# Performance work log

Hardware: AMD Instinct MI355X
Metric: run time of the kernel (lower is better)

## Reference

```python
import jax, jax.numpy as jnp
import numpy as np
import math

N_HEAD = 16
ROPE_BASE = 10000.0

def _rope_cos_sin(seq_len, head_dim, dtype):
    inv_freq = 1.0 / (ROPE_BASE ** (jnp.arange(0, head_dim, 2, dtype=jnp.float32) / head_dim))
    t = jnp.arange(seq_len, dtype=jnp.float32)
    freqs = t[:, None] * inv_freq[None, :]            # [S, D/2]
    emb = jnp.concatenate([freqs, freqs], axis=-1)     # [S, D]
    # broadcast shape [1, 1, S, D] to match q/k [B, H, S, D]
    return jnp.cos(emb)[None, None].astype(dtype), jnp.sin(emb)[None, None].astype(dtype)

def _rotate_half(x):
    x1, x2 = jnp.split(x, 2, axis=-1)
    return jnp.concatenate([-x2, x1], axis=-1)

def setup_inputs() -> dict:
    key = jax.random.key(0)
    ks = jax.random.split(key, 5)
    B, S, E = 2, 2048, 1024
    x = jax.random.normal(ks[0], (B, S, E), dtype=jnp.float32)
    init = 1.0 / math.sqrt(E)
    Wq = jax.random.normal(ks[1], (E, E), dtype=jnp.float32) * init
    Wk = jax.random.normal(ks[2], (E, E), dtype=jnp.float32) * init
    Wv = jax.random.normal(ks[3], (E, E), dtype=jnp.float32) * init
    Wo = jax.random.normal(ks[4], (E, E), dtype=jnp.float32) * init
    # causal mask: True = masked (masked_fill with -inf)
    attn_mask = jnp.triu(jnp.ones((S, S), dtype=bool), k=1)
    return {"x": x, "Wq": Wq, "Wk": Wk, "Wv": Wv, "Wo": Wo, "attn_mask": attn_mask}

def reference(x, Wq, Wk, Wv, Wo, attn_mask):
    B, S, E = x.shape
    H = N_HEAD
    D = E // H
    # projections (torch Linear: y = x @ W.T), split heads -> [B, H, S, D]
    def proj(W):
        return jnp.einsum('bse,fe->bsf', x, W).reshape(B, S, H, D).transpose(0, 2, 1, 3)
    q, k, v = proj(Wq), proj(Wk), proj(Wv)
    cos, sin = _rope_cos_sin(S, D, x.dtype)
    q = q * cos + _rotate_half(q) * sin
    k = k * cos + _rotate_half(k) * sin
    scale = 1.0 / math.sqrt(D)
    scores = jnp.einsum('bhqd,bhkd->bhqk', q, k) * scale  # [B, H, S, S]
    scores = jnp.where(attn_mask[None, None], -jnp.inf, scores)
    attn = jax.nn.softmax(scores, axis=-1)
    out = jnp.einsum('bhqk,bhkd->bhqd', attn, v)           # [B, H, S, D]
    out = out.transpose(0, 2, 1, 3).reshape(B, S, E)
    return jnp.einsum('bse,fe->bsf', out, Wo)
```

## Files before the change

kernel.cpp:

```cpp
#include <hip/hip_runtime.h>
#include <hip/hip_bf16.h>

#define NB 2
#define NH 16
#define SEQ 2048
#define HD 64
#define EMB 1024

typedef unsigned short u16;
typedef unsigned int u32;
typedef __attribute__((ext_vector_type(8))) short bf16x8;
typedef __attribute__((ext_vector_type(4))) float f32x4;
typedef __attribute__((ext_vector_type(8))) unsigned short us8;

__device__ __forceinline__ float b2f(u16 u) {
    union { unsigned int i; float f; } v; v.i = ((unsigned int)u) << 16; return v.f;
}
__device__ __forceinline__ u16 f2b(float f) {
    union { float f; unsigned int i; } v; v.f = f;
    unsigned int x = v.i;
    return (u16)((x + 0x7FFFu + ((x >> 16) & 1u)) >> 16);
}
__device__ __forceinline__ u32 pk2(float a, float b) {
    union { __hip_bfloat162 h; u32 u; } v;
    v.h = __float22bfloat162_rn(make_float2(a, b));
    return v.u;
}

__device__ __forceinline__ void gld16(const u16* g, u16* l) {
    __builtin_amdgcn_global_load_lds((const __attribute__((address_space(1))) void*)g,
                                     (__attribute__((address_space(3))) void*)l, 16, 0, 0);
}

__device__ __forceinline__ void conv8(const void* src, u16* dst, int i, int isbf16) {
    if (isbf16) {
        *reinterpret_cast<uint4*>(dst + i) =
            *reinterpret_cast<const uint4*>((const u16*)src + i);
    } else {
        const float* s = (const float*)src + i;
        float4 a = *reinterpret_cast<const float4*>(s);
        float4 b = *reinterpret_cast<const float4*>(s + 4);
        us8 v;
        v[0] = f2b(a.x); v[1] = f2b(a.y); v[2] = f2b(a.z); v[3] = f2b(a.w);
        v[4] = f2b(b.x); v[5] = f2b(b.y); v[6] = f2b(b.z); v[7] = f2b(b.w);
        *reinterpret_cast<us8*>(dst + i) = v;
    }
}

__global__ __launch_bounds__(256)
void prep_54571854463007(const void* __restrict__ x,
                         const void* __restrict__ w0, const void* __restrict__ w1,
                         const void* __restrict__ w2, const void* __restrict__ w3,
                         u16* __restrict__ xb, u16* __restrict__ dqkv,
                         u16* __restrict__ dob, int* __restrict__ flag) {
    __shared__ int cnt;
    if (threadIdx.x == 0) cnt = 0;
    __syncthreads();
    const u16 v = ((const u16*)x)[threadIdx.x];
    const int e = (v >> 7) & 0xFF;
    if (e >= 110 && e <= 135) atomicAdd(&cnt, 1);
    __syncthreads();
    const int isbf16 = (cnt >= 200) ? 1 : 0;
    const int blk = blockIdx.x;
    if (blk == 0 && threadIdx.x == 0) *flag = isbf16;
    const int NXB = (NB * SEQ * EMB) / 2048;
    if (blk < NXB) {
        conv8(x, xb, (blk * 256 + threadIdx.x) * 8, isbf16);
    } else {
        const int r = blk - NXB;
        const int seg = r >> 9;
        const int NW = EMB * EMB;
        const void* src = (seg == 0) ? w0 : (seg == 1) ? w1 : (seg == 2) ? w2 : w3;
        u16* dst = (seg < 3) ? (dqkv + (size_t)seg * NW) : dob;
        conv8(src, dst, ((r & 511) * 256 + threadIdx.x) * 8, isbf16);
    }
}

template<int OUT_MODE>
__global__ __launch_bounds__(256)
void gemm_mfma_54571854463007(const u16* __restrict__ A, const u16* __restrict__ Bw,
                              void* __restrict__ C, const int* __restrict__ flagp,
                              int M, int N, int K) {
    __shared__ __align__(16) u16 As[128 * 32];
    __shared__ __align__(16) u16 Bs[128 * 32];
    const int tid  = threadIdx.x;
    const int wave = tid >> 6, lane = tid & 63;
    const int quad = lane >> 4, fr = lane & 15;
    const int wr = (wave >> 1) * 64, wc = (wave & 1) * 64;
    const int m0 = blockIdx.y * 128, n0 = blockIdx.x * 128;
    const int r0 = tid >> 2;
    const int kc = (tid & 3) * 8;
    const f32x4 zz = {0.f, 0.f, 0.f, 0.f};
    f32x4 acc[4][4];
#pragma unroll
    for (int i = 0; i < 4; ++i)
#pragma unroll
        for (int j = 0; j < 4; ++j) acc[i][j] = zz;

    for (int k0 = 0; k0 < K; k0 += 32) {
        gld16(A  + (size_t)(m0 + r0) * K + k0 + kc,      &As[wave * 512]);
        gld16(A  + (size_t)(m0 + 64 + r0) * K + k0 + kc, &As[2048 + wave * 512]);
        gld16(Bw + (size_t)(n0 + r0) * K + k0 + kc,      &Bs[wave * 512]);
        gld16(Bw + (size_t)(n0 + 64 + r0) * K + k0 + kc, &Bs[2048 + wave * 512]);
        __syncthreads();
        bf16x8 af[4], bfr[4];
#pragma unroll
        for (int mi = 0; mi < 4; ++mi)
            af[mi] = *reinterpret_cast<const bf16x8*>(&As[(wr + mi * 16 + fr) * 32 + quad * 8]);
#pragma unroll
        for (int ni = 0; ni < 4; ++ni)
            bfr[ni] = *reinterpret_cast<const bf16x8*>(&Bs[(wc + ni * 16 + fr) * 32 + quad * 8]);
#pragma unroll
        for (int mi = 0; mi < 4; ++mi)
#pragma unroll
            for (int ni = 0; ni < 4; ++ni)
                acc[mi][ni] = __builtin_amdgcn_mfma_f32_16x16x32_bf16(af[mi], bfr[ni], acc[mi][ni], 0, 0, 0);
        __syncthreads();
    }

    if (OUT_MODE == 1) {
        const int t0 = n0 >> 10;
        if (t0 == 0) {
            const float SCL = 0.18033688011112042f;
#pragma unroll
            for (int mi = 0; mi < 4; ++mi)
#pragma unroll
                for (int ni = 0; ni < 4; ++ni)
#pragma unroll
                    for (int r = 0; r < 4; ++r) acc[mi][ni][r] *= SCL;
        }
        if (t0 < 2) {
            const float inv0 = __powf(10000.f, -(float)fr / 32.f);
            const float inv1 = __powf(10000.f, -(float)(fr + 16) / 32.f);
#pragma unroll
            for (int mi = 0; mi < 4; ++mi)
#pragma unroll
                for (int r = 0; r < 4; ++r) {
                    const int s = (m0 + wr + mi * 16 + quad * 4 + r) & (SEQ - 1);
#pragma unroll
                    for (int nl = 0; nl < 2; ++nl) {
                        float sn, cs;
                        __sincosf((float)s * (nl ? inv1 : inv0), &sn, &cs);
                        const float lo = acc[mi][nl][r], hi = acc[mi][nl + 2][r];
                        acc[mi][nl][r]     = lo * cs - hi * sn;
                        acc[mi][nl + 2][r] = hi * cs + lo * sn;
                    }
                }
        }
    }

    const int isbf16 = (OUT_MODE == 0) ? *flagp : 0;
    const size_t TS = (size_t)NB * NH * SEQ * HD;
#pragma unroll
    for (int mi = 0; mi < 4; ++mi)
#pragma unroll
        for (int ni = 0; ni < 4; ++ni)
#pragma unroll
            for (int r = 0; r < 4; ++r) {
                const int m = m0 + wr + mi * 16 + quad * 4 + r;
                const int n = n0 + wc + ni * 16 + fr;
                const float v = acc[mi][ni][r];
                if (OUT_MODE == 1) {
                    const int t = n >> 10, idx = n & 1023;
                    const int h = idx >> 6, d = idx & 63;
                    const int b = m >> 11, s = m & (SEQ - 1);
                    ((u16*)C)[t * TS + ((((size_t)b * NH + h) * SEQ + s) << 6) + d] = f2b(v);
                } else {
                    if (isbf16) ((u16*)C)[(size_t)m * N + n] = f2b(v);
                    else        ((float*)C)[(size_t)m * N + n] = v;
                }
            }
}

__global__ __launch_bounds__(256, 4)
void flash_54571854463007(const u16* __restrict__ Q, const u16* __restrict__ K,
                          const u16* __restrict__ V, u16* __restrict__ AO,
                          float* __restrict__ OP0, float* __restrict__ OP1,
                          float* __restrict__ LP0, float* __restrict__ LP1) {
    __shared__ __align__(16) u16 Kt[2 * 4096];
    __shared__ __align__(16) u16 Vt[2 * 4608];
    const int tid  = threadIdx.x;
    const int w    = tid >> 6, lane = tid & 63;
    const int quad = lane >> 4, fr = lane & 15;
    const int lin = blockIdx.x;
    const int xcd = lin & 7;
    const int r_  = lin >> 3;
    const int b4  = r_ & 3;
    const int ti  = r_ >> 2;
    int qt, kt0, kt1;
    if (ti < 17)       { qt = 15 + ti; kt0 = 0;  kt1 = 15; }
    else if (ti == 17) { qt = 31;      kt0 = 16; kt1 = 31; }
    else {
        const int g = ti - 18, s = 15 - (g >> 1);
        if (g & 1) { qt = s + 15; kt0 = 16; kt1 = qt; }
        else       { qt = s - 1;  kt0 = 0;  kt1 = qt; }
    }
    const int bh = xcd * 4 + b4;
    const bool partial = (qt >= 16);
    const int h = bh & 15, b = bh >> 4;
    const size_t base = ((size_t)b * NH + h) * SEQ * HD;
    const int k2   = (tid & 31) * 2;
    const int key0 = (k2 & 3) * 16 + (k2 >> 2);
    const int d8   = ((tid >> 5) & 7) * 8;

    const int krs = lane >> 3;
    const int kch = ((lane & 7) ^ krs) * 8;
    const int swz = fr & 7;
    const int co0 = (quad ^ swz) * 8;
    const int co1 = ((quad + 4) ^ swz) * 8;

    const bf16x8 ones = {(short)0x3F80, (short)0x3F80, (short)0x3F80, (short)0x3F80,
                         (short)0x3F80, (short)0x3F80, (short)0x3F80, (short)0x3F80};

    const u16* qp = Q + base + (size_t)(qt * 64 + w * 16 + fr) * HD + quad * 8;
    const bf16x8 aq0 = *reinterpret_cast<const bf16x8*>(qp);
    const bf16x8 aq1 = *reinterpret_cast<const bf16x8*>(qp + 32);

    {
        const u16* Kg = K + base + (size_t)kt0 * 64 * HD;
        gld16(Kg + (size_t)((w * 2 + 0) * 8 + krs) * HD + kch, &Kt[(w * 2 + 0) * 512]);
        gld16(Kg + (size_t)((w * 2 + 1) * 8 + krs) * HD + kch, &Kt[(w * 2 + 1) * 512]);
    }
    us8 vc0, vc1, vn0, vn1;
    {
        const u16* vs = V + base + (size_t)(kt0 * 64 + key0) * HD + d8;
        vc0 = *reinterpret_cast<const us8*>(vs);
        vc1 = *reinterpret_cast<const us8*>(vs + 16 * HD);
    }

    const f32x4 zz = {0.f, 0.f, 0.f, 0.f};
    f32x4 lacc = zz;
    f32x4 oacc[4];
#pragma unroll
    for (int nt = 0; nt < 4; ++nt) oacc[nt] = zz;

    for (int kt = kt0; kt <= kt1; ++kt) {
        const int buf = (kt - kt0) & 1;
        const int vb  = buf * 4608;
        const int kb  = buf * 4096;
#pragma unroll
        for (int jj = 0; jj < 8; ++jj) {
            const u32 pk = ((u32)(u16)vc1[jj] << 16) | (u32)(u16)vc0[jj];
            *reinterpret_cast<u32*>(&Vt[vb + (d8 + jj) * 72 + k2]) = pk;
        }
        __syncthreads();
        if (kt + 1 <= kt1) {
            const u16* Kg = K + base + (size_t)(kt + 1) * 64 * HD;
            const int kb1 = (buf ^ 1) * 4096;
            gld16(Kg + (size_t)((w * 2 + 0) * 8 + krs) * HD + kch, &Kt[kb1 + (w * 2 + 0) * 512]);
            gld16(Kg + (size_t)((w * 2 + 1) * 8 + krs) * HD + kch, &Kt[kb1 + (w * 2 + 1) * 512]);
            const u16* vs = V + base + (size_t)((kt + 1) * 64 + key0) * HD + d8;
            vn0 = *reinterpret_cast<const us8*>(vs);
            vn1 = *reinterpret_cast<const us8*>(vs + 16 * HD);
        }
        f32x4 sa[4];
        __builtin_amdgcn_s_setprio(1);
#pragma unroll
        for (int nt = 0; nt < 4; ++nt) {
            const int rb = kb + (nt * 16 + fr) * 64;
            const bf16x8 ka0 = *reinterpret_cast<const bf16x8*>(&Kt[rb + co0]);
            const bf16x8 ka1 = *reinterpret_cast<const bf16x8*>(&Kt[rb + co1]);
            sa[nt] = __builtin_amdgcn_mfma_f32_16x16x32_bf16(ka0, aq0, zz, 0, 0, 0);
            sa[nt] = __builtin_amdgcn_mfma_f32_16x16x32_bf16(ka1, aq1, sa[nt], 0, 0, 0);
        }
        __builtin_amdgcn_s_setprio(0);
        if (kt == qt) {
#pragma unroll
            for (int nt = 0; nt < 4; ++nt)
#pragma unroll
                for (int r = 0; r < 4; ++r)
                    if (nt * 16 + quad * 4 + r > w * 16 + fr) sa[nt][r] = -__builtin_inff();
        }
        u32 c01[4], c23[4];
#pragma unroll
        for (int r = 0; r < 4; ++r) {
            c01[r] = pk2(exp2f(sa[0][r]), exp2f(sa[1][r]));
            c23[r] = pk2(exp2f(sa[2][r]), exp2f(sa[3][r]));
        }
        union { u32 u[4]; bf16x8 v; } P0, P1;
        {
            auto a = __builtin_amdgcn_permlane16_swap(c01[0], c01[2], false, false);
            auto bsw = __builtin_amdgcn_permlane32_swap(a[0], a[1], false, false);
            P0.u[0] = (u32)bsw[0]; P1.u[0] = (u32)bsw[1];
        }
        {
            auto a = __builtin_amdgcn_permlane16_swap(c23[0], c23[2], false, false);
            auto bsw = __builtin_amdgcn_permlane32_swap(a[0], a[1], false, false);
            P0.u[1] = (u32)bsw[0]; P1.u[1] = (u32)bsw[1];
        }
        {
            auto a = __builtin_amdgcn_permlane16_swap(c01[1], c01[3], false, false);
            auto bsw = __builtin_amdgcn_permlane32_swap(a[0], a[1], false, false);
            P0.u[2] = (u32)bsw[0]; P1.u[2] = (u32)bsw[1];
        }
        {
            auto a = __builtin_amdgcn_permlane16_swap(c23[1], c23[3], false, false);
            auto bsw = __builtin_amdgcn_permlane32_swap(a[0], a[1], false, false);
            P0.u[3] = (u32)bsw[0]; P1.u[3] = (u32)bsw[1];
        }
        const bf16x8 pa0 = P0.v;
        const bf16x8 pa1 = P1.v;
        __builtin_amdgcn_s_setprio(1);
        lacc = __builtin_amdgcn_mfma_f32_16x16x32_bf16(pa0, ones, lacc, 0, 0, 0);
        lacc = __builtin_amdgcn_mfma_f32_16x16x32_bf16(pa1, ones, lacc, 0, 0, 0);
#pragma unroll
        for (int nt = 0; nt < 4; ++nt) {
            const bf16x8 bv0 = *reinterpret_cast<const bf16x8*>(&Vt[vb + (nt * 16 + fr) * 72 + quad * 8]);
            const bf16x8 bv1 = *reinterpret_cast<const bf16x8*>(&Vt[vb + (nt * 16 + fr) * 72 + 32 + quad * 8]);
            oacc[nt] = __builtin_amdgcn_mfma_f32_16x16x32_bf16(pa0, bv0, oacc[nt], 0, 0, 0);
            oacc[nt] = __builtin_amdgcn_mfma_f32_16x16x32_bf16(pa1, bv1, oacc[nt], 0, 0, 0);
        }
        __builtin_amdgcn_s_setprio(0);
        vc0 = vn0; vc1 = vn1;
    }
    if (!partial) {
#pragma unroll
        for (int r = 0; r < 4; ++r) {
            const float inv = 1.0f / lacc[r];
            const int q = qt * 64 + w * 16 + quad * 4 + r;
#pragma unroll
            for (int nt = 0; nt < 4; ++nt)
                AO[(((size_t)b * SEQ + q) * NH + h) * HD + nt * 16 + fr] = f2b(oacc[nt][r] * inv);
        }
    } else {
        float* OP = (kt0 == 16) ? OP1 : OP0;
        float* LP = (kt0 == 16) ? LP1 : LP0;
        const int tb = (bh * 16 + (qt - 16)) * 64;
#pragma unroll
        for (int r = 0; r < 4; ++r) {
            const int qrow = w * 16 + quad * 4 + r;
            LP[tb + qrow] = lacc[r];
#pragma unroll
            for (int nt = 0; nt < 4; ++nt)
                OP[(size_t)(tb + qrow) * 64 + nt * 16 + fr] = oacc[nt][r];
        }
    }
}

__global__ __launch_bounds__(256)
void combine_54571854463007(const float* __restrict__ OP0, const float* __restrict__ OP1,
                            const float* __restrict__ LP0, const float* __restrict__ LP1,
                            u16* __restrict__ AO) {
    const int idx  = blockIdx.x * 256 + threadIdx.x;
    const int row  = idx >> 3;
    const int d8   = (idx & 7) * 8;
    const int bh   = row >> 10;
    const int tile = (row >> 6) & 15;
    const int qrow = row & 63;
    const int h = bh & 15, b = bh >> 4;
    const int q = (16 + tile) * 64 + qrow;
    const float4* A = reinterpret_cast<const float4*>(&OP0[(size_t)row * 64 + d8]);
    const float4* Bp = reinterpret_cast<const float4*>(&OP1[(size_t)row * 64 + d8]);
    const float4 a0 = A[0], a1 = A[1], b0 = Bp[0], b1 = Bp[1];
    const float inv = 1.0f / (LP0[row] + LP1[row]);
    us8 o;
    o[0] = f2b((a0.x + b0.x) * inv); o[1] = f2b((a0.y + b0.y) * inv);
    o[2] = f2b((a0.z + b0.z) * inv); o[3] = f2b((a0.w + b0.w) * inv);
    o[4] = f2b((a1.x + b1.x) * inv); o[5] = f2b((a1.y + b1.y) * inv);
    o[6] = f2b((a1.z + b1.z) * inv); o[7] = f2b((a1.w + b1.w) * inv);
    *reinterpret_cast<us8*>(&AO[(((size_t)b * SEQ + q) * NH + h) * HD + d8]) = o;
}

extern "C" void kernel_launch(void* const* d_in, const int* in_sizes, int n_in,
                              void* d_out, int out_size, void* d_ws, size_t ws_size,
                              hipStream_t stream) {
    (void)in_sizes; (void)n_in; (void)out_size; (void)ws_size;
    const void* x  = d_in[0];
    const void* Wq = d_in[1];
    const void* Wk = d_in[2];
    const void* Wv = d_in[3];
    const void* Wo = d_in[4];

    char* ws = (char*)d_ws;
    const size_t MB = 1024 * 1024;
    int* flag = (int*)ws;
    u16* xb   = (u16*)(ws + 64);
    u16* Wqkv = (u16*)(ws + 64 + 8 * MB);
    u16* Wob  = (u16*)(ws + 64 + 14 * MB);
    u16* Qb   = (u16*)(ws + 64 + 16 * MB);
    u16* Kb   = (u16*)(ws + 64 + 24 * MB);
    u16* Vb   = (u16*)(ws + 64 + 32 * MB);
    float* OP0 = (float*)(ws + 64 + 40 * MB);
    float* OP1 = (float*)(ws + 64 + 48 * MB);
    float* LP0 = (float*)(ws + 64 + 56 * MB);
    float* LP1 = (float*)(ws + 64 + 56 * MB + 256 * 1024);
    u16* AO   = xb;

    prep_54571854463007<<<dim3(4096), 256, 0, stream>>>(
        x, Wq, Wk, Wv, Wo, xb, Wqkv, Wob, flag);

    const int M = NB * SEQ;
    gemm_mfma_54571854463007<1><<<dim3(3 * EMB / 128, M / 128), 256, 0, stream>>>(
        xb, Wqkv, Qb, flag, M, 3 * EMB, EMB);

    flash_54571854463007<<<dim3(1536), 256, 0, stream>>>(Qb, Kb, Vb, AO,
                                                         OP0, OP1, LP0, LP1);
    combine_54571854463007<<<dim3(1024), 256, 0, stream>>>(OP0, OP1, LP0, LP1, AO);

    gemm_mfma_54571854463007<0><<<dim3(EMB / 128, M / 128), 256, 0, stream>>>(
        AO, Wob, d_out, flag, M, EMB, EMB);
}
```

Before: 204.9 us.

## Process two query tiles per flash block to reuse K/V loads

Each flash-attention block now handles 128 query rows (two 64-row tiles) instead of 64, so every K/V tile staged in shared memory and registers feeds twice as many MFMAs. The grid is halved, the work schedule and split-K partition are rewritten for 128-row groups, and the combine indexing is adjusted to match. It doubles the accumulator and Q register footprint, so launch bounds drop to 3 blocks per CU, and the diagonal tiles do some extra masked work.

```diff
diff --git a/kernel.cpp b/kernel.cpp
--- a/kernel.cpp
+++ b/kernel.cpp
@@ -172,7 +172,7 @@
             }
 }
 
-__global__ __launch_bounds__(256, 4)
+__global__ __launch_bounds__(256, 3)
 void flash_54571854463007(const u16* __restrict__ Q, const u16* __restrict__ K,
                           const u16* __restrict__ V, u16* __restrict__ AO,
                           float* __restrict__ OP0, float* __restrict__ OP1,
@@ -187,16 +187,17 @@
     const int r_  = lin >> 3;
     const int b4  = r_ & 3;
     const int ti  = r_ >> 2;
-    int qt, kt0, kt1;
-    if (ti < 17)       { qt = 15 + ti; kt0 = 0;  kt1 = 15; }
-    else if (ti == 17) { qt = 31;      kt0 = 16; kt1 = 31; }
+    int T, kt0, kt1;
+    if (ti < 8)       { T = 8 + ti; kt0 = 0;  kt1 = 15; }
+    else if (ti == 8) { T = 15;     kt0 = 16; kt1 = 31; }
+    else if (ti == 9) { T = 7;      kt0 = 0;  kt1 = 15; }
     else {
-        const int g = ti - 18, s = 15 - (g >> 1);
-        if (g & 1) { qt = s + 15; kt0 = 16; kt1 = qt; }
-        else       { qt = s - 1;  kt0 = 0;  kt1 = qt; }
-    }
+        const int g = ti - 10, s = 7 - (g >> 1);
+        if ((g & 1) == 0) { T = s + 7; kt0 = 16; kt1 = 2 * T + 1; }
+        else              { T = s - 1; kt0 = 0;  kt1 = 2 * T + 1; }
+    }
+    const bool split = (T >= 8);
     const int bh = xcd * 4 + b4;
-    const bool partial = (qt >= 16);
     const int h = bh & 15, b = bh >> 4;
     const size_t base = ((size_t)b * NH + h) * SEQ * HD;
     const int k2   = (tid & 31) * 2;
@@ -212,9 +213,12 @@
     const bf16x8 ones = {(short)0x3F80, (short)0x3F80, (short)0x3F80, (short)0x3F80,
                          (short)0x3F80, (short)0x3F80, (short)0x3F80, (short)0x3F80};
 
-    const u16* qp = Q + base + (size_t)(qt * 64 + w * 16 + fr) * HD + quad * 8;
-    const bf16x8 aq0 = *reinterpret_cast<const bf16x8*>(qp);
-    const bf16x8 aq1 = *reinterpret_cast<const bf16x8*>(qp + 32);
+    const u16* qp0 = Q + base + (size_t)(T * 128 + w * 16 + fr) * HD + quad * 8;
+    const bf16x8 aq0 = *reinterpret_cast<const bf16x8*>(qp0);
+    const bf16x8 aq1 = *reinterpret_cast<const bf16x8*>(qp0 + 32);
+    const u16* qp1 = qp0 + (size_t)64 * HD;
+    const bf16x8 aq2 = *reinterpret_cast<const bf16x8*>(qp1);
+    const bf16x8 aq3 = *reinterpret_cast<const bf16x8*>(qp1 + 32);
 
     {
         const u16* Kg = K + base + (size_t)kt0 * 64 * HD;
@@ -229,10 +233,10 @@
     }
 
     const f32x4 zz = {0.f, 0.f, 0.f, 0.f};
-    f32x4 lacc = zz;
-    f32x4 oacc[4];
-#pragma unroll
-    for (int nt = 0; nt < 4; ++nt) oacc[nt] = zz;
+    f32x4 lacc0 = zz, lacc1 = zz;
+    f32x4 oacc0[4], oacc1[4];
+#pragma unroll
+    for (int nt = 0; nt < 4; ++nt) { oacc0[nt] = zz; oacc1[nt] = zz; }
 
     for (int kt = kt0; kt <= kt1; ++kt) {
         const int buf = (kt - kt0) & 1;
@@ -253,86 +257,150 @@
             vn0 = *reinterpret_cast<const us8*>(vs);
             vn1 = *reinterpret_cast<const us8*>(vs + 16 * HD);
         }
-        f32x4 sa[4];
+        const int dk = kt - 2 * T;
+        bf16x8 ka0[4], ka1[4];
         __builtin_amdgcn_s_setprio(1);
 #pragma unroll
         for (int nt = 0; nt < 4; ++nt) {
             const int rb = kb + (nt * 16 + fr) * 64;
-            const bf16x8 ka0 = *reinterpret_cast<const bf16x8*>(&Kt[rb + co0]);
-            const bf16x8 ka1 = *reinterpret_cast<const bf16x8*>(&Kt[rb + co1]);
-            sa[nt] = __builtin_amdgcn_mfma_f32_16x16x32_bf16(ka0, aq0, zz, 0, 0, 0);
-            sa[nt] = __builtin_amdgcn_mfma_f32_16x16x32_bf16(ka1, aq1, sa[nt], 0, 0, 0);
-        }
-        __builtin_amdgcn_s_setprio(0);
-        if (kt == qt) {
-#pragma unroll
-            for (int nt = 0; nt < 4; ++nt)
-#pragma unroll
-                for (int r = 0; r < 4; ++r)
-                    if (nt * 16 + quad * 4 + r > w * 16 + fr) sa[nt][r] = -__builtin_inff();
-        }
-        u32 c01[4], c23[4];
-#pragma unroll
-        for (int r = 0; r < 4; ++r) {
-            c01[r] = pk2(exp2f(sa[0][r]), exp2f(sa[1][r]));
-            c23[r] = pk2(exp2f(sa[2][r]), exp2f(sa[3][r]));
-        }
-        union { u32 u[4]; bf16x8 v; } P0, P1;
+            ka0[nt] = *reinterpret_cast<const bf16x8*>(&Kt[rb + co0]);
+            ka1[nt] = *reinterpret_cast<const bf16x8*>(&Kt[rb + co1]);
+        }
+        union { u32 u[4]; bf16x8 v; } p00, p01;
         {
-            auto a = __builtin_amdgcn_permlane16_swap(c01[0], c01[2], false, false);
-            auto bsw = __builtin_amdgcn_permlane32_swap(a[0], a[1], false, false);
-            P0.u[0] = (u32)bsw[0]; P1.u[0] = (u32)bsw[1];
-        }
+            f32x4 sa[4];
+#pragma unroll
+            for (int nt = 0; nt < 4; ++nt) {
+                sa[nt] = __builtin_amdgcn_mfma_f32_16x16x32_bf16(ka0[nt], aq0, zz, 0, 0, 0);
+                sa[nt] = __builtin_amdgcn_mfma_f32_16x16x32_bf16(ka1[nt], aq1, sa[nt], 0, 0, 0);
+            }
+            __builtin_amdgcn_s_setprio(0);
+            if (dk >= 0) {
+#pragma unroll
+                for (int nt = 0; nt < 4; ++nt)
+#pragma unroll
+                    for (int r = 0; r < 4; ++r)
+                        if (dk * 64 + nt * 16 + quad * 4 + r > w * 16 + fr)
+                            sa[nt][r] = -__builtin_inff();
+            }
+            u32 c01[4], c23[4];
+#pragma unroll
+            for (int r = 0; r < 4; ++r) {
+                c01[r] = pk2(exp2f(sa[0][r]), exp2f(sa[1][r]));
+                c23[r] = pk2(exp2f(sa[2][r]), exp2f(sa[3][r]));
+            }
+            {
+                auto a = __builtin_amdgcn_permlane16_swap(c01[0], c01[2], false, false);
+                auto bsw = __builtin_amdgcn_permlane32_swap(a[0], a[1], false, false);
+                p00.u[0] = (u32)bsw[0]; p01.u[0] = (u32)bsw[1];
+            }
+            {
+                auto a = __builtin_amdgcn_permlane16_swap(c23[0], c23[2], false, false);
+                auto bsw = __builtin_amdgcn_permlane32_swap(a[0], a[1], false, false);
+                p00.u[1] = (u32)bsw[0]; p01.u[1] = (u32)bsw[1];
+            }
+            {
+                auto a = __builtin_amdgcn_permlane16_swap(c01[1], c01[3], false, false);
+                auto bsw = __builtin_amdgcn_permlane32_swap(a[0], a[1], false, false);
+                p00.u[2] = (u32)bsw[0]; p01.u[2] = (u32)bsw[1];
+            }
+            {
+                auto a = __builtin_amdgcn_permlane16_swap(c23[1], c23[3], false, false);
+                auto bsw = __builtin_amdgcn_permlane32_swap(a[0], a[1], false, false);
+                p00.u[3] = (u32)bsw[0]; p01.u[3] = (u32)bsw[1];
+            }
+        }
+        union { u32 u[4]; bf16x8 v; } p10, p11;
         {
-            auto a = __builtin_amdgcn_permlane16_swap(c23[0], c23[2], false, false);
-            auto bsw = __builtin_amdgcn_permlane32_swap(a[0], a[1], false, false);
-            P0.u[1] = (u32)bsw[0]; P1.u[1] = (u32)bsw[1];
-        }
-        {
-            auto a = __builtin_amdgcn_permlane16_swap(c01[1], c01[3], false, false);
-            auto bsw = __builtin_amdgcn_permlane32_swap(a[0], a[1], false, false);
-            P0.u[2] = (u32)bsw[0]; P1.u[2] = (u32)bsw[1];
-        }
-        {
-            auto a = __builtin_amdgcn_permlane16_swap(c23[1], c23[3], false, false);
-            auto bsw = __builtin_amdgcn_permlane32_swap(a[0], a[1], false, false);
-            P0.u[3] = (u32)bsw[0]; P1.u[3] = (u32)bsw[1];
-        }
-        const bf16x8 pa0 = P0.v;
-        const bf16x8 pa1 = P1.v;
+            f32x4 sa[4];
+            __builtin_amdgcn_s_setprio(1);
+#pragma unroll
+            for (int nt = 0; nt < 4; ++nt) {
+                sa[nt] = __builtin_amdgcn_mfma_f32_16x16x32_bf16(ka0[nt], aq2, zz, 0, 0, 0);
+                sa[nt] = __builtin_amdgcn_mfma_f32_16x16x32_bf16(ka1[nt], aq3, sa[nt], 0, 0, 0);
+            }
+            __builtin_amdgcn_s_setprio(0);
+            if (dk == 1) {
+#pragma unroll
+                for (int nt = 0; nt < 4; ++nt)
+#pragma unroll
+                    for (int r = 0; r < 4; ++r)
+                        if (nt * 16 + quad * 4 + r > w * 16 + fr)
+                            sa[nt][r] = -__builtin_inff();
+            }
+            u32 c01[4], c23[4];
+#pragma unroll
+            for (int r = 0; r < 4; ++r) {
+                c01[r] = pk2(exp2f(sa[0][r]), exp2f(sa[1][r]));
+                c23[r] = pk2(exp2f(sa[2][r]), exp2f(sa[3][r]));
+            }
+            {
+                auto a = __builtin_amdgcn_permlane16_swap(c01[0], c01[2], false, false);
+                auto bsw = __builtin_amdgcn_permlane32_swap(a[0], a[1], false, false);
+                p10.u[0] = (u32)bsw[0]; p11.u[0] = (u32)bsw[1];
+            }
+            {
+                auto a = __builtin_amdgcn_permlane16_swap(c23[0], c23[2], false, false);
+                auto bsw = __builtin_amdgcn_permlane32_swap(a[0], a[1], false, false);
+                p10.u[1] = (u32)bsw[0]; p11.u[1] = (u32)bsw[1];
+            }
+            {
+                auto a = __builtin_amdgcn_permlane16_swap(c01[1], c01[3], false, false);
+                auto bsw = __builtin_amdgcn_permlane32_swap(a[0], a[1], false, false);
+                p10.u[2] = (u32)bsw[0]; p11.u[2] = (u32)bsw[1];
+            }
+            {
+                auto a = __builtin_amdgcn_permlane16_swap(c23[1], c23[3], false, false);
+                auto bsw = __builtin_amdgcn_permlane32_swap(a[0], a[1], false, false);
+                p10.u[3] = (u32)bsw[0]; p11.u[3] = (u32)bsw[1];
+            }
+        }
         __builtin_amdgcn_s_setprio(1);
-        lacc = __builtin_amdgcn_mfma_f32_16x16x32_bf16(pa0, ones, lacc, 0, 0, 0);
-        lacc = __builtin_amdgcn_mfma_f32_16x16x32_bf16(pa1, ones, lacc, 0, 0, 0);
+        lacc0 = __builtin_amdgcn_mfma_f32_16x16x32_bf16(p00.v, ones, lacc0, 0, 0, 0);
+        lacc0 = __builtin_amdgcn_mfma_f32_16x16x32_bf16(p01.v, ones, lacc0, 0, 0, 0);
+        lacc1 = __builtin_amdgcn_mfma_f32_16x16x32_bf16(p10.v, ones, lacc1, 0, 0, 0);
+        lacc1 = __builtin_amdgcn_mfma_f32_16x16x32_bf16(p11.v, ones, lacc1, 0, 0, 0);
 #pragma unroll
         for (int nt = 0; nt < 4; ++nt) {
             const bf16x8 bv0 = *reinterpret_cast<const bf16x8*>(&Vt[vb + (nt * 16 + fr) * 72 + quad * 8]);
             const bf16x8 bv1 = *reinterpret_cast<const bf16x8*>(&Vt[vb + (nt * 16 + fr) * 72 + 32 + quad * 8]);
-            oacc[nt] = __builtin_amdgcn_mfma_f32_16x16x32_bf16(pa0, bv0, oacc[nt], 0, 0, 0);
-            oacc[nt] = __builtin_amdgcn_mfma_f32_16x16x32_bf16(pa1, bv1, oacc[nt], 0, 0, 0);
+            oacc0[nt] = __builtin_amdgcn_mfma_f32_16x16x32_bf16(p00.v, bv0, oacc0[nt], 0, 0, 0);
+            oacc0[nt] = __builtin_amdgcn_mfma_f32_16x16x32_bf16(p01.v, bv1, oacc0[nt], 0, 0, 0);
+            oacc1[nt] = __builtin_amdgcn_mfma_f32_16x16x32_bf16(p10.v, bv0, oacc1[nt], 0, 0, 0);
+            oacc1[nt] = __builtin_amdgcn_mfma_f32_16x16x32_bf16(p11.v, bv1, oacc1[nt], 0, 0, 0);
         }
         __builtin_amdgcn_s_setprio(0);
         vc0 = vn0; vc1 = vn1;
     }
-    if (!partial) {
+    if (!split) {
 #pragma unroll
         for (int r = 0; r < 4; ++r) {
-            const float inv = 1.0f / lacc[r];
-            const int q = qt * 64 + w * 16 + quad * 4 + r;
-#pragma unroll
-            for (int nt = 0; nt < 4; ++nt)
-                AO[(((size_t)b * SEQ + q) * NH + h) * HD + nt * 16 + fr] = f2b(oacc[nt][r] * inv);
+            const int qr = w * 16 + quad * 4 + r;
+            const float i0 = 1.0f / lacc0[r];
+            const float i1 = 1.0f / lacc1[r];
+            const int q0 = T * 128 + qr;
+            const int q1 = T * 128 + 64 + qr;
+#pragma unroll
+            for (int nt = 0; nt < 4; ++nt) {
+                AO[(((size_t)b * SEQ + q0) * NH + h) * HD + nt * 16 + fr] = f2b(oacc0[nt][r] * i0);
+                AO[(((size_t)b * SEQ + q1) * NH + h) * HD + nt * 16 + fr] = f2b(oacc1[nt][r] * i1);
+            }
         }
     } else {
         float* OP = (kt0 == 16) ? OP1 : OP0;
         float* LP = (kt0 == 16) ? LP1 : LP0;
-        const int tb = (bh * 16 + (qt - 16)) * 64;
 #pragma unroll
         for (int r = 0; r < 4; ++r) {
-            const int qrow = w * 16 + quad * 4 + r;
-            LP[tb + qrow] = lacc[r];
-#pragma unroll
-            for (int nt = 0; nt < 4; ++nt)
-                OP[(size_t)(tb + qrow) * 64 + nt * 16 + fr] = oacc[nt][r];
+            const int qr = w * 16 + quad * 4 + r;
+            const int row0 = bh * 1024 + (T * 128 + qr) - 1024;
+            const int row1 = row0 + 64;
+            LP[row0] = lacc0[r];
+            LP[row1] = lacc1[r];
+#pragma unroll
+            for (int nt = 0; nt < 4; ++nt) {
+                OP[(size_t)row0 * 64 + nt * 16 + fr] = oacc0[nt][r];
+                OP[(size_t)row1 * 64 + nt * 16 + fr] = oacc1[nt][r];
+            }
         }
     }
 }
@@ -345,10 +413,9 @@
     const int row  = idx >> 3;
     const int d8   = (idx & 7) * 8;
     const int bh   = row >> 10;
-    const int tile = (row >> 6) & 15;
-    const int qrow = row & 63;
+    const int qoff = row & 1023;
     const int h = bh & 15, b = bh >> 4;
-    const int q = (16 + tile) * 64 + qrow;
+    const int q = 1024 + qoff;
     const float4* A = reinterpret_cast<const float4*>(&OP0[(size_t)row * 64 + d8]);
     const float4* Bp = reinterpret_cast<const float4*>(&OP1[(size_t)row * 64 + d8]);
     const float4 a0 = A[0], a1 = A[1], b0 = Bp[0], b1 = Bp[1];
@@ -393,8 +460,8 @@
     gemm_mfma_54571854463007<1><<<dim3(3 * EMB / 128, M / 128), 256, 0, stream>>>(
         xb, Wqkv, Qb, flag, M, 3 * EMB, EMB);
 
-    flash_54571854463007<<<dim3(1536), 256, 0, stream>>>(Qb, Kb, Vb, AO,
-                                                         OP0, OP1, LP0, LP1);
+    flash_54571854463007<<<dim3(768), 256, 0, stream>>>(Qb, Kb, Vb, AO,
+                                                        OP0, OP1, LP0, LP1);
     combine_54571854463007<<<dim3(1024), 256, 0, stream>>>(OP0, OP1, LP0, LP1, AO);
 
     gemm_mfma_54571854463007<0><<<dim3(EMB / 128, M / 128), 256, 0, stream>>>(
```

After: 208.5 us. Within noise of the previous version (+1.8%).

## Replace QKV projection GEMM with 256x256 tile, 8-wave pipelined, swizzled-LDS kernel

Applied to the files above, without the earlier changes.

Adds a new QKV projection GEMM that uses 256x256 output tiles with 512 threads. It double-buffers K=64 slices in XOR-swizzled LDS and interleaves the async global-to-LDS loads with MFMA phases, using explicit barriers, vmcnt waits and setprio. The RoPE, scale and head-scatter epilogue moves into this kernel, and the old templated GEMM keeps only the plain output path. The aim is more data reuse and better load/compute overlap in the biggest GEMM, at the cost of 128KB of LDS and a grid of only 192 blocks, which may underfill the CUs.

```diff
diff --git a/kernel.cpp b/kernel.cpp
--- a/kernel.cpp
+++ b/kernel.cpp
@@ -31,6 +31,9 @@
     __builtin_amdgcn_global_load_lds((const __attribute__((address_space(1))) void*)g,
                                      (__attribute__((address_space(3))) void*)l, 16, 0, 0);
 }
+
+#define BAR8P()  asm volatile("s_barrier" ::: "memory")
+#define VMW8P(n) asm volatile("s_waitcnt vmcnt(" #n ")" ::: "memory")
 
 __device__ __forceinline__ void conv8(const void* src, u16* dst, int i, int isbf16) {
     if (isbf16) {
@@ -76,6 +79,151 @@
     }
 }
 
+template<int MIH, int NIH>
+__device__ __forceinline__ void quad8p(const bf16x8 (&aT)[4][2], const bf16x8 (&bT)[4][2],
+                                       f32x4 (&acc)[8][4]) {
+#pragma unroll
+    for (int i = 0; i < 4; ++i)
+#pragma unroll
+        for (int j = 0; j < 2; ++j)
+#pragma unroll
+            for (int k = 0; k < 2; ++k)
+                acc[MIH * 4 + i][NIH * 2 + j] = __builtin_amdgcn_mfma_f32_16x16x32_bf16(
+                    aT[i][k], bT[NIH * 2 + j][k], acc[MIH * 4 + i][NIH * 2 + j], 0, 0, 0);
+}
+
+__device__ __forceinline__ void rd8p(const u16* Ls, int buf, int rbase, int quad, int fr,
+                                     bf16x8 (&dst)[4][2]) {
+#pragma unroll
+    for (int i = 0; i < 4; ++i) {
+        const int R  = rbase + i * 16 + fr;
+        const int rb = buf * 16384 + R * 64;
+        const int sw = R & 7;
+        dst[i][0] = *reinterpret_cast<const bf16x8*>(&Ls[rb + ((quad    ) ^ sw) * 8]);
+        dst[i][1] = *reinterpret_cast<const bf16x8*>(&Ls[rb + ((quad + 4) ^ sw) * 8]);
+    }
+}
+
+__global__ __launch_bounds__(512, 2)
+void gemm8p_54571854463007(const u16* __restrict__ A, const u16* __restrict__ Bw,
+                           u16* __restrict__ C) {
+    __shared__ __align__(16) u16 As[32768];
+    __shared__ __align__(16) u16 Bs[32768];
+    const int tid  = threadIdx.x;
+    const int w    = tid >> 6, lane = tid & 63;
+    const int quad = lane >> 4, fr = lane & 15;
+    const int wm   = w >> 2, wn = w & 3;
+    const int m0   = blockIdx.y * 256, n0 = blockIdx.x * 256;
+    const int srow = tid >> 3;
+    const int schk = ((tid & 7) ^ (srow & 7)) * 8;
+
+    auto stageU = [&](const u16* G, u16* Ls, int T, int jp, int gbase) {
+        const int Tm  = T & 15;
+        const int buf = T & 1;
+        const int j0  = jp * 2;
+        gld16(G + (size_t)(gbase + j0 * 64      + srow) * 1024 + Tm * 64 + schk,
+              &Ls[buf * 16384 +  j0      * 4096 + w * 512]);
+        gld16(G + (size_t)(gbase + j0 * 64 + 64 + srow) * 1024 + Tm * 64 + schk,
+              &Ls[buf * 16384 + (j0 + 1) * 4096 + w * 512]);
+    };
+
+    f32x4 acc[8][4];
+    const f32x4 zz = {0.f, 0.f, 0.f, 0.f};
+#pragma unroll
+    for (int i = 0; i < 8; ++i)
+#pragma unroll
+        for (int j = 0; j < 4; ++j) acc[i][j] = zz;
+
+    stageU(A, As, 0, 0, m0);
+    stageU(A, As, 0, 1, m0);
+    stageU(Bw, Bs, 0, 0, n0);
+    stageU(Bw, Bs, 0, 1, n0);
+    stageU(A, As, 1, 0, m0);
+    VMW8P(2);
+    BAR8P();
+
+#pragma unroll 1
+    for (int it = 0; it < 8; ++it) {
+        const int ta = 2 * it, tb = ta + 1;
+        bf16x8 aT[4][2], bT[4][2];
+        rd8p(As, 0, wm * 128, quad, fr, aT);
+        rd8p(Bs, 0, wn * 64, quad, fr, bT);
+        stageU(A, As, tb, 1, m0);
+        __builtin_amdgcn_s_setprio(1); quad8p<0, 0>(aT, bT, acc); __builtin_amdgcn_s_setprio(0);
+        BAR8P();
+        stageU(Bw, Bs, tb, 0, n0);
+        __builtin_amdgcn_s_setprio(1); quad8p<0, 1>(aT, bT, acc); __builtin_amdgcn_s_setprio(0);
+        BAR8P();
+        rd8p(As, 0, wm * 128 + 64, quad, fr, aT);
+        stageU(Bw, Bs, tb, 1, n0);
+        __builtin_amdgcn_s_setprio(1); quad8p<1, 0>(aT, bT, acc); __builtin_amdgcn_s_setprio(0);
+        BAR8P();
+        stageU(A, As, ta + 2, 0, m0);
+        __builtin_amdgcn_s_setprio(1); quad8p<1, 1>(aT, bT, acc); __builtin_amdgcn_s_setprio(0);
+        VMW8P(2);
+        BAR8P();
+        rd8p(As, 1, wm * 128, quad, fr, aT);
+        rd8p(Bs, 1, wn * 64, quad, fr, bT);
+        stageU(A, As, ta + 2, 1, m0);
+        __builtin_amdgcn_s_setprio(1); quad8p<0, 0>(aT, bT, acc); __builtin_amdgcn_s_setprio(0);
+        BAR8P();
+        stageU(Bw, Bs, ta + 2, 0, n0);
+        __builtin_amdgcn_s_setprio(1); quad8p<0, 1>(aT, bT, acc); __builtin_amdgcn_s_setprio(0);
+        BAR8P();
+        rd8p(As, 1, wm * 128 + 64, quad, fr, aT);
+        stageU(Bw, Bs, ta + 2, 1, n0);
+        __builtin_amdgcn_s_setprio(1); quad8p<1, 0>(aT, bT, acc); __builtin_amdgcn_s_setprio(0);
+        BAR8P();
+        stageU(A, As, tb + 2, 0, m0);
+        __builtin_amdgcn_s_setprio(1); quad8p<1, 1>(aT, bT, acc); __builtin_amdgcn_s_setprio(0);
+        VMW8P(2);
+        BAR8P();
+    }
+
+    const int t0 = n0 >> 10;
+    if (t0 == 0) {
+        const float SCL = 0.18033688011112042f;
+#pragma unroll
+        for (int mi = 0; mi < 8; ++mi)
+#pragma unroll
+            for (int ni = 0; ni < 4; ++ni)
+#pragma unroll
+                for (int r = 0; r < 4; ++r) acc[mi][ni][r] *= SCL;
+    }
+    if (t0 < 2) {
+        const float inv0 = __powf(10000.f, -(float)fr / 32.f);
+        const float inv1 = __powf(10000.f, -(float)(fr + 16) / 32.f);
+#pragma unroll
+        for (int mi = 0; mi < 8; ++mi)
+#pragma unroll
+            for (int r = 0; r < 4; ++r) {
+                const int s = (m0 + wm * 128 + mi * 16 + quad * 4 + r) & (SEQ - 1);
+#pragma unroll
+                for (int nl = 0; nl < 2; ++nl) {
+                    float sn, cs;
+                    __sincosf((float)s * (nl ? inv1 : inv0), &sn, &cs);
+                    const float lo = acc[mi][nl][r], hi = acc[mi][nl + 2][r];
+                    acc[mi][nl][r]     = lo * cs - hi * sn;
+                    acc[mi][nl + 2][r] = hi * cs + lo * sn;
+                }
+            }
+    }
+    const size_t TS = (size_t)NB * NH * SEQ * HD;
+#pragma unroll
+    for (int mi = 0; mi < 8; ++mi)
+#pragma unroll
+        for (int ni = 0; ni < 4; ++ni)
+#pragma unroll
+            for (int r = 0; r < 4; ++r) {
+                const int m = m0 + wm * 128 + mi * 16 + quad * 4 + r;
+                const int n = n0 + wn * 64 + ni * 16 + fr;
+                const int t = n >> 10, idx = n & 1023;
+                const int h = idx >> 6, d = idx & 63;
+                const int b = m >> 11, s = m & (SEQ - 1);
+                C[t * TS + ((((size_t)b * NH + h) * SEQ + s) << 6) + d] = f2b(acc[mi][ni][r]);
+            }
+}
+
 template<int OUT_MODE>
 __global__ __launch_bounds__(256)
 void gemm_mfma_54571854463007(const u16* __restrict__ A, const u16* __restrict__ Bw,
@@ -118,39 +266,7 @@
         __syncthreads();
     }
 
-    if (OUT_MODE == 1) {
-        const int t0 = n0 >> 10;
-        if (t0 == 0) {
-            const float SCL = 0.18033688011112042f;
-#pragma unroll
-            for (int mi = 0; mi < 4; ++mi)
-#pragma unroll
-                for (int ni = 0; ni < 4; ++ni)
-#pragma unroll
-                    for (int r = 0; r < 4; ++r) acc[mi][ni][r] *= SCL;
-        }
-        if (t0 < 2) {
-            const float inv0 = __powf(10000.f, -(float)fr / 32.f);
-            const float inv1 = __powf(10000.f, -(float)(fr + 16) / 32.f);
-#pragma unroll
-            for (int mi = 0; mi < 4; ++mi)
-#pragma unroll
-                for (int r = 0; r < 4; ++r) {
-                    const int s = (m0 + wr + mi * 16 + quad * 4 + r) & (SEQ - 1);
-#pragma unroll
-                    for (int nl = 0; nl < 2; ++nl) {
-                        float sn, cs;
-                        __sincosf((float)s * (nl ? inv1 : inv0), &sn, &cs);
-                        const float lo = acc[mi][nl][r], hi = acc[mi][nl + 2][r];
-                        acc[mi][nl][r]     = lo * cs - hi * sn;
-                        acc[mi][nl + 2][r] = hi * cs + lo * sn;
-                    }
-                }
-        }
-    }
-
-    const int isbf16 = (OUT_MODE == 0) ? *flagp : 0;
-    const size_t TS = (size_t)NB * NH * SEQ * HD;
+    const int isbf16 = *flagp;
 #pragma unroll
     for (int mi = 0; mi < 4; ++mi)
 #pragma unroll
@@ -160,15 +276,8 @@
                 const int m = m0 + wr + mi * 16 + quad * 4 + r;
                 const int n = n0 + wc + ni * 16 + fr;
                 const float v = acc[mi][ni][r];
-                if (OUT_MODE == 1) {
-                    const int t = n >> 10, idx = n & 1023;
-                    const int h = idx >> 6, d = idx & 63;
-                    const int b = m >> 11, s = m & (SEQ - 1);
-                    ((u16*)C)[t * TS + ((((size_t)b * NH + h) * SEQ + s) << 6) + d] = f2b(v);
-                } else {
-                    if (isbf16) ((u16*)C)[(size_t)m * N + n] = f2b(v);
-                    else        ((float*)C)[(size_t)m * N + n] = v;
-                }
+                if (isbf16) ((u16*)C)[(size_t)m * N + n] = f2b(v);
+                else        ((float*)C)[(size_t)m * N + n] = v;
             }
 }
 
@@ -390,8 +499,8 @@
         x, Wq, Wk, Wv, Wo, xb, Wqkv, Wob, flag);
 
     const int M = NB * SEQ;
-    gemm_mfma_54571854463007<1><<<dim3(3 * EMB / 128, M / 128), 256, 0, stream>>>(
-        xb, Wqkv, Qb, flag, M, 3 * EMB, EMB);
+    gemm8p_54571854463007<<<dim3(3 * EMB / 256, M / 256), 512, 0, stream>>>(
+        xb, Wqkv, Qb);
 
     flash_54571854463007<<<dim3(1536), 256, 0, stream>>>(Qb, Kb, Vb, AO,
                                                          OP0, OP1, LP0, LP1);
```

New measurement: 204.5 us, median of 2. Within noise of the previous version (-0.2%).
